# Optimization experiments

Hardware: AMD Instinct MI355X
Metric: run time of the kernel (lower is better)

Reference implementation:

```python
import jax, jax.numpy as jnp
import numpy as np

V = 50257; CTX = 2048; D = 1024; H = 16; L = 8; DH = D // H
B = 2; S = 2048; EPS = 1e-5


def setup_inputs() -> dict:
    key = jax.random.key(0)
    ks = jax.random.split(key, 8)
    s = 0.02
    def n(k, shape):
        return jax.random.normal(k, shape, jnp.float32) * s
    return {
        "x": jax.random.randint(ks[0], (B, S), 0, V),
        "wte": n(ks[1], (V, D)),
        "wpe": n(ks[2], (CTX, D)),
        "ln1_g": jnp.ones((L, D), jnp.float32), "ln1_b": jnp.zeros((L, D), jnp.float32),
        "w_qkv": n(ks[3], (L, D, 3 * D)), "b_qkv": jnp.zeros((L, 3 * D), jnp.float32),
        "w_proj": n(ks[4], (L, D, D)), "b_proj": jnp.zeros((L, D), jnp.float32),
        "ln2_g": jnp.ones((L, D), jnp.float32), "ln2_b": jnp.zeros((L, D), jnp.float32),
        "w_fc": n(ks[5], (L, D, 4 * D)), "b_fc": jnp.zeros((L, 4 * D), jnp.float32),
        "w_cp": n(ks[6], (L, 4 * D, D)), "b_cp": jnp.zeros((L, D), jnp.float32),
        "lnf_g": jnp.ones((D,), jnp.float32), "lnf_b": jnp.zeros((D,), jnp.float32),
        "w_head": n(ks[7], (D, V)),
    }


def layernorm(x, g, b):
    m = x.mean(-1, keepdims=True)
    v = ((x - m) ** 2).mean(-1, keepdims=True)
    return (x - m) * jax.lax.rsqrt(v + EPS) * g + b


def gpt_forward(x, wte, wpe, ln1_g, ln1_b, w_qkv, b_qkv, w_proj, b_proj,
                ln2_g, ln2_b, w_fc, b_fc, w_cp, b_cp, lnf_g, lnf_b, w_head):
    Bx, Sx = x.shape
    h = wte[x] + wpe[:Sx]                       # [B,S,D]
    mask = jnp.tril(jnp.ones((Sx, Sx), bool))   # causal mask
    scale = DH ** -0.5

    def block(h, p):
        g1, b1, wq, bq, wp, bp, g2, b2, wf, bf, wc, bc = p
        y = layernorm(h, g1, b1)
        qkv = y @ wq + bq                        # [B,S,3D]
        q, k, v = jnp.split(qkv, 3, axis=-1)
        q = q.reshape(Bx, Sx, H, DH)
        k = k.reshape(Bx, Sx, H, DH)
        v = v.reshape(Bx, Sx, H, DH)
        att = jnp.einsum('bqhd,bkhd->bhqk', q, k) * scale
        att = jnp.where(mask, att, -jnp.inf)
        att = jax.nn.softmax(att, axis=-1)
        z = jnp.einsum('bhqk,bkhd->bqhd', att, v).reshape(Bx, Sx, D)
        h = h + z @ wp + bp
        y2 = layernorm(h, g2, b2)
        h = h + jax.nn.gelu(y2 @ wf + bf, approximate=False) @ wc + bc
        return h, None

    h, _ = jax.lax.scan(block, h, (ln1_g, ln1_b, w_qkv, b_qkv, w_proj, b_proj,
                                   ln2_g, ln2_b, w_fc, b_fc, w_cp, b_cp))
    h = layernorm(h, lnf_g, lnf_b)
    logits = h[:, -1:, :] @ w_head              # [B,1,V] (last position only)
    return logits


def reference(x, wte, wpe, ln1_g, ln1_b, w_qkv, b_qkv, w_proj, b_proj,
              ln2_g, ln2_b, w_fc, b_fc, w_cp, b_cp, lnf_g, lnf_b, w_head):
    return gpt_forward(x, wte, wpe, ln1_g, ln1_b, w_qkv, b_qkv, w_proj, b_proj,
                       ln2_g, ln2_b, w_fc, b_fc, w_cp, b_cp, lnf_g, lnf_b, w_head)
```

## Files before the change

### kernel.cpp

```cpp
#include <hip/hip_runtime.h>
#include <hip/hip_bf16.h>
#include <math.h>

#define VOCAB 50257
#define CTX 2048
#define DMODEL 1024
#define NHEAD 16
#define NLAYER 8
#define DHEAD 64
#define BATCH 2
#define SEQ 2048
#define NTOK (BATCH * SEQ)

typedef __bf16 bf16x8 __attribute__((ext_vector_type(8)));
typedef float  f32x4  __attribute__((ext_vector_type(4)));
typedef unsigned short ushort4v __attribute__((ext_vector_type(4)));
typedef unsigned short ushort8v __attribute__((ext_vector_type(8)));

__device__ inline void gl_lds16(const void* g, void* l) {
    __builtin_amdgcn_global_load_lds(
        (const __attribute__((address_space(1))) unsigned int*)g,
        (__attribute__((address_space(3))) unsigned int*)l, 16, 0, 0);
}

__device__ inline unsigned short f2bs(float v) {
    __hip_bfloat16 t = __float2bfloat16(v);
    return *(unsigned short*)&t;
}

__device__ void embed_body(int t, const int* __restrict__ x,
                           const float* __restrict__ wte,
                           const float* __restrict__ wpe,
                           float* __restrict__ h) {
    int s = t & (SEQ - 1);
    int tok = x[t];
    const float* pe = wpe + (long)s * DMODEL;
    const float* te = wte + (long)tok * DMODEL;
    float* ph = h + (long)t * DMODEL;
    for (int d = threadIdx.x; d < DMODEL; d += 256)
        ph[d] = te[d] + pe[d];
}

__device__ inline float wave_sum(float v) {
    for (int off = 32; off; off >>= 1) v += __shfl_xor(v, off);
    return v;
}

__global__ void ln_wave(const float* __restrict__ in, unsigned short* __restrict__ out,
                        const float* __restrict__ g, const float* __restrict__ b) {
    const int w = threadIdx.x >> 6, lane = threadIdx.x & 63;
    const int row = blockIdx.x * 4 + w;
    const float* px = in + (long)row * DMODEL;
    f32x4 x[4];
    float s = 0.f;
    #pragma unroll
    for (int i = 0; i < 4; ++i) {
        x[i] = *(const f32x4*)&px[i * 256 + lane * 4];
        s += x[i][0] + x[i][1] + x[i][2] + x[i][3];
    }
    s = wave_sum(s);
    const float mean = s * (1.0f / DMODEL);
    float s2 = 0.f;
    #pragma unroll
    for (int i = 0; i < 4; ++i)
        #pragma unroll
        for (int j = 0; j < 4; ++j) { float d = x[i][j] - mean; s2 += d * d; }
    s2 = wave_sum(s2);
    const float r = 1.0f / sqrtf(s2 * (1.0f / DMODEL) + 1e-5f);
    unsigned short* po = out + (long)row * DMODEL;
    #pragma unroll
    for (int i = 0; i < 4; ++i) {
        const int d0 = i * 256 + lane * 4;
        f32x4 gv = *(const f32x4*)&g[d0];
        f32x4 bv = *(const f32x4*)&b[d0];
        ushort4v pk;
        #pragma unroll
        for (int j = 0; j < 4; ++j)
            pk[j] = f2bs((x[i][j] - mean) * r * gv[j] + bv[j]);
        *(ushort4v*)&po[d0] = pk;
    }
}

__global__ void ln_final(const float* __restrict__ in, float* __restrict__ out,
                         const float* __restrict__ g, const float* __restrict__ b,
                         long row_stride) {
    __shared__ float red[4], red2[4];
    int row = blockIdx.x;
    const float* px = in + (long)row * row_stride;
    float* po = out + (long)row * DMODEL;
    int tid = threadIdx.x;
    int wid = tid >> 6, lane = tid & 63;
    float x[4];
    float s = 0.f;
    #pragma unroll
    for (int i = 0; i < 4; ++i) { x[i] = px[tid + i * 256]; s += x[i]; }
    s = wave_sum(s);
    if (lane == 0) red[wid] = s;
    __syncthreads();
    float mean = (red[0] + red[1] + red[2] + red[3]) * (1.0f / DMODEL);
    float s2 = 0.f;
    #pragma unroll
    for (int i = 0; i < 4; ++i) { float d = x[i] - mean; s2 += d * d; }
    s2 = wave_sum(s2);
    if (lane == 0) red2[wid] = s2;
    __syncthreads();
    float var = (red2[0] + red2[1] + red2[2] + red2[3]) * (1.0f / DMODEL);
    float r = 1.0f / sqrtf(var + 1e-5f);
    #pragma unroll
    for (int i = 0; i < 4; ++i) {
        int d = tid + i * 256;
        po[d] = (x[i] - mean) * r * g[d] + b[d];
    }
}

__device__ void convT_body(char* smem, int kx, int ny, const float* __restrict__ W,
                           unsigned short* __restrict__ WT, int K, int N) {
    float (*t)[65] = (float(*)[65])smem;
    const int k0 = kx * 64, n0 = ny * 64;
    const int tid = threadIdx.x;
    {
        const int krow = tid >> 4, c4 = (tid & 15) * 4;
        #pragma unroll
        for (int p = 0; p < 4; ++p) {
            f32x4 gv = *(const f32x4*)&W[(long)(k0 + p * 16 + krow) * N + n0 + c4];
            #pragma unroll
            for (int j = 0; j < 4; ++j) t[p * 16 + krow][c4 + j] = gv[j];
        }
    }
    __syncthreads();
    {
        const int n = tid >> 3, kl = (tid & 7) * 8;
        #pragma unroll
        for (int p = 0; p < 2; ++p) {
            ushort8v pk;
            #pragma unroll
            for (int j = 0; j < 8; ++j) pk[j] = f2bs(t[kl + j][p * 32 + n]);
            *(ushort8v*)&WT[(long)(n0 + p * 32 + n) * K + k0 + kl] = pk;
        }
    }
}

__device__ void convT_body512(char* smem, int kx, int ny, const float* __restrict__ W,
                              unsigned short* __restrict__ WT, int K, int N) {
    float (*t)[65] = (float(*)[65])smem;
    const int k0 = kx * 64, n0 = ny * 64;
    const int tid = threadIdx.x;
    {
        const int krow = tid >> 4, c4 = (tid & 15) * 4;
        #pragma unroll
        for (int p = 0; p < 2; ++p) {
            f32x4 gv = *(const f32x4*)&W[(long)(k0 + p * 32 + krow) * N + n0 + c4];
            #pragma unroll
            for (int j = 0; j < 4; ++j) t[p * 32 + krow][c4 + j] = gv[j];
        }
    }
    __syncthreads();
    {
        const int n = tid >> 3, kl = (tid & 7) * 8;
        ushort8v pk;
        #pragma unroll
        for (int j = 0; j < 8; ++j) pk[j] = f2bs(t[kl + j][n]);
        *(ushort8v*)&WT[(long)(n0 + n) * K + k0 + kl] = pk;
    }
}

#define STG_A(KS, H) do { \
    const unsigned short* g_ = A + (long)(bm + (H) * 128 + srow) * K + (KS) * 64 + stgch; \
    unsigned short* s_ = LDS + (((KS) & 1) * 2 + (H)) * 8192 + (w * 8) * 64; \
    gl_lds16(g_, s_); gl_lds16(g_ + 64L * K, s_ + 4096); \
} while (0)
#define STG_B(KS, H) do { \
    const unsigned short* g_ = BT + (long)(bn + (H) * 128 + srow) * K + (KS) * 64 + stgch; \
    unsigned short* s_ = LDS + 32768 + (((KS) & 1) * 2 + (H)) * 8192 + (w * 8) * 64; \
    gl_lds16(g_, s_); gl_lds16(g_ + 64L * K, s_ + 4096); \
} while (0)
#define MM2(M_, x0, x1) do { \
    acc[M_][0] = __builtin_amdgcn_mfma_f32_16x16x32_bf16(x0, bfr[0], acc[M_][0], 0, 0, 0); \
    acc[M_][0] = __builtin_amdgcn_mfma_f32_16x16x32_bf16(x1, bfr[1], acc[M_][0], 0, 0, 0); \
    acc[M_][1] = __builtin_amdgcn_mfma_f32_16x16x32_bf16(x0, bfr[2], acc[M_][1], 0, 0, 0); \
    acc[M_][1] = __builtin_amdgcn_mfma_f32_16x16x32_bf16(x1, bfr[3], acc[M_][1], 0, 0, 0); \
    acc[M_][2] = __builtin_amdgcn_mfma_f32_16x16x32_bf16(x0, bfr[4], acc[M_][2], 0, 0, 0); \
    acc[M_][2] = __builtin_amdgcn_mfma_f32_16x16x32_bf16(x1, bfr[5], acc[M_][2], 0, 0, 0); \
    acc[M_][3] = __builtin_amdgcn_mfma_f32_16x16x32_bf16(x0, bfr[6], acc[M_][3], 0, 0, 0); \
    acc[M_][3] = __builtin_amdgcn_mfma_f32_16x16x32_bf16(x1, bfr[7], acc[M_][3], 0, 0, 0); \
} while (0)
#define PHASE(Q, SPAR, STAGE_STMT, TAIL_STMT) do { \
    bf16x8 a00, a01, a10, a11; \
    if (((Q) & 3) == 0) { \
        const unsigned short* Bb_ = lBp[SPAR] + ((wc & 1) * 64 + fr) * 64; \
        bfr[0] = *(const bf16x8*)(Bb_ + rd0);        bfr[1] = *(const bf16x8*)(Bb_ + rd1); \
        bfr[2] = *(const bf16x8*)(Bb_ + 1024 + rd0); bfr[3] = *(const bf16x8*)(Bb_ + 1024 + rd1); \
        bfr[4] = *(const bf16x8*)(Bb_ + 2048 + rd0); bfr[5] = *(const bf16x8*)(Bb_ + 2048 + rd1); \
        bfr[6] = *(const bf16x8*)(Bb_ + 3072 + rd0); bfr[7] = *(const bf16x8*)(Bb_ + 3072 + rd1); \
    } \
    { const unsigned short* Ab_ = lAp[SPAR] + fr * 64; \
      a00 = *(const bf16x8*)(Ab_ + (((Q) & 3) * 2) * 1024 + rd0); \
      a01 = *(const bf16x8*)(Ab_ + (((Q) & 3) * 2) * 1024 + rd1); \
      a10 = *(const bf16x8*)(Ab_ + (((Q) & 3) * 2 + 1) * 1024 + rd0); \
      a11 = *(const bf16x8*)(Ab_ + (((Q) & 3) * 2 + 1) * 1024 + rd1); } \
    STAGE_STMT; \
    __builtin_amdgcn_s_barrier(); \
    asm volatile("s_waitcnt lgkmcnt(0)" ::: "memory"); \
    __builtin_amdgcn_sched_barrier(0); \
    __builtin_amdgcn_s_setprio(1); \
    MM2(((Q) & 3) * 2, a00, a01); \
    MM2(((Q) & 3) * 2 + 1, a10, a11); \
    __builtin_amdgcn_s_setprio(0); \
    TAIL_STMT; \
    __builtin_amdgcn_s_barrier(); \
} while (0)

template<int EPI>
__global__ __launch_bounds__(512, 1)
void mm_mfma256(const unsigned short* __restrict__ A,
                const unsigned short* __restrict__ BT,
                const float* __restrict__ bias,
                void* __restrict__ Cout, int M, int N, int K, int nbx) {
    extern __shared__ unsigned short LDS[];
    const int tid = threadIdx.x;
    const int w = tid >> 6, lane = tid & 63;
    const int wr = w >> 2, wc = w & 3;
    const int nwg = gridDim.x, bid = blockIdx.x;
    const int swz = (bid & 7) * (nwg >> 3) + (bid >> 3);
    const int bm = (swz / nbx) * 256, bn = (swz % nbx) * 256;

    f32x4 acc[8][4];
    #pragma unroll
    for (int m = 0; m < 8; ++m)
        #pragma unroll
        for (int n = 0; n < 4; ++n)
            acc[m][n] = (f32x4){0.f, 0.f, 0.f, 0.f};

    const int fr = lane & 15, kg = lane >> 4;
    const int rd0 = 8 * (kg ^ (lane & 7)), rd1 = 8 * ((kg + 4) ^ (lane & 7));
    const int stgch = 8 * ((lane & 7) ^ (lane >> 3));
    const int srow = w * 8 + (lane >> 3);
    unsigned short* const lAp[2] = { LDS + wr * 8192, LDS + (2 + wr) * 8192 };
    unsigned short* const lBp[2] = { LDS + 32768 + (wc >> 1) * 8192,
                                     LDS + 32768 + (2 + (wc >> 1)) * 8192 };
    bf16x8 bfr[8];

    STG_B(0, 0); STG_B(0, 1); STG_A(0, 0); STG_A(0, 1); STG_B(1, 0); STG_B(1, 1);
    asm volatile("s_waitcnt vmcnt(4)" ::: "memory");
    __builtin_amdgcn_sched_barrier(0);
    __builtin_amdgcn_s_barrier();

    const int T = K >> 7;
    for (int t = 0; t < T; ++t) {
        const int s = 2 * t;
        const bool nl = (t < T - 1);
        PHASE(0, 0, STG_A(s + 1, 0), );
        PHASE(1, 0, STG_A(s + 1, 1), );
        PHASE(2, 0, if (nl) STG_B(s + 2, 0), );
        PHASE(3, 0, if (nl) STG_B(s + 2, 1),
              if (nl) { asm volatile("s_waitcnt vmcnt(4)" ::: "memory"); } else { asm volatile("s_waitcnt vmcnt(0)" ::: "memory"); } __builtin_amdgcn_sched_barrier(0); );
        PHASE(4, 1, if (nl) STG_A(s + 2, 0), );
        PHASE(5, 1, if (nl) STG_A(s + 2, 1), );
        PHASE(6, 1, if (nl) STG_B(s + 3, 0), );
        PHASE(7, 1, if (nl) STG_B(s + 3, 1),
              if (nl) { asm volatile("s_waitcnt vmcnt(4)" ::: "memory"); __builtin_amdgcn_sched_barrier(0); } );
    }

    const int r0 = (lane >> 4) * 4;
    #pragma unroll
    for (int n = 0; n < 4; ++n) {
        int colb = bn + wc * 64 + n * 16;
        float bv = bias[colb + fr];
        #pragma unroll
        for (int m = 0; m < 8; ++m) {
            int rowb = bm + wr * 128 + m * 16 + r0;
            if (EPI == 3) {
                unsigned short* qkvB = (unsigned short*)Cout;
                int which = colb >> 10, hh = (colb & 1023) >> 6, dbase = colb & 63;
                int b_ = rowb >> 11, s_ = rowb & 2047;
                long bh2 = b_ * 16 + hh;
                float v[4];
                #pragma unroll
                for (int r = 0; r < 4; ++r) v[r] = acc[m][n][r] + bv;
                if (which == 2) {
                    ushort4v pk;
                    #pragma unroll
                    for (int r = 0; r < 4; ++r) pk[r] = f2bs(v[r]);
                    *(ushort4v*)&qkvB[8388608L + (bh2 * 64 + dbase + fr) * 2048 + s_] = pk;
                } else {
                    unsigned short* dst = qkvB + (long)which * 4194304L +
                                          (bh2 * 2048 + s_) * 64 + dbase + fr;
                    #pragma unroll
                    for (int r = 0; r < 4; ++r) dst[r * 64] = f2bs(v[r]);
                }
            } else {
                #pragma unroll
                for (int r = 0; r < 4; ++r) {
                    long row = rowb + r, col = colb + fr;
                    float v = acc[m][n][r] + bv;
                    v = 0.5f * v * (1.0f + erff(v * 0.70710678118f));
                    ((__hip_bfloat16*)Cout)[row * N + col] = __float2bfloat16(v);
                }
            }
        }
    }
}

__device__ void n64_body(char* smem, int bx, int by,
                         const unsigned short* __restrict__ A,
                         const unsigned short* __restrict__ BT,
                         const float* __restrict__ bias, const float* __restrict__ R,
                         float* __restrict__ Cout, int M, int N, int K) {
    unsigned short* As = (unsigned short*)smem;
    unsigned short* Bs = As + 2 * 128 * 32;
    const int tid = threadIdx.x;
    const int w = tid >> 6, lane = tid & 63;
    const int bm = by * 128, bn = bx * 64;
    const int wr = (w >> 1) * 64, wc = (w & 1) * 32;

    f32x4 acc[4][2];
    #pragma unroll
    for (int m = 0; m < 4; ++m)
        #pragma unroll
        for (int n = 0; n < 2; ++n)
            acc[m][n] = (f32x4){0.f, 0.f, 0.f, 0.f};

    const int lrow = lane >> 2;
    const int lcol = (lane & 3) * 8;
    const unsigned short* gA = A + (long)(bm + w * 32 + lrow) * K + lcol;
    const unsigned short* gB = BT + (long)(bn + w * 16 + lrow) * K + lcol;

#define N64_STAGE(K0, BB) do { \
    gl_lds16(gA + (K0),          &As[(BB) * 4096 + (w * 32) * 32]); \
    gl_lds16(gA + (K0) + 16 * K, &As[(BB) * 4096 + (w * 32 + 16) * 32]); \
    gl_lds16(gB + (K0),          &Bs[(BB) * 2048 + (w * 16) * 32]); \
} while (0)

    N64_STAGE(0, 0);

    const int T = K >> 5;
    for (int t = 0; t < T; ++t) {
        const int buf = t & 1;
        if (t + 1 < T) {
            N64_STAGE((t + 1) * 32, buf ^ 1);
            asm volatile("s_waitcnt vmcnt(3)" ::: "memory");
        } else {
            asm volatile("s_waitcnt vmcnt(0)" ::: "memory");
        }
        __builtin_amdgcn_sched_barrier(0);
        __builtin_amdgcn_s_barrier();

        bf16x8 a[4], b[2];
        #pragma unroll
        for (int m = 0; m < 4; ++m)
            a[m] = *(const bf16x8*)&As[buf * 4096 + (wr + m * 16 + (lane & 15)) * 32 + (lane >> 4) * 8];
        #pragma unroll
        for (int n = 0; n < 2; ++n)
            b[n] = *(const bf16x8*)&Bs[buf * 2048 + (wc + n * 16 + (lane & 15)) * 32 + (lane >> 4) * 8];
        #pragma unroll
        for (int m = 0; m < 4; ++m)
            #pragma unroll
            for (int n = 0; n < 2; ++n)
                acc[m][n] = __builtin_amdgcn_mfma_f32_16x16x32_bf16(a[m], b[n], acc[m][n], 0, 0, 0);

        __builtin_amdgcn_s_barrier();
    }
#undef N64_STAGE

    const int r0 = (lane >> 4) * 4, cc = lane & 15;
    #pragma unroll
    for (int n = 0; n < 2; ++n) {
        int colb = bn + wc + n * 16;
        float bv = bias[colb + cc];
        #pragma unroll
        for (int m = 0; m < 4; ++m) {
            int rowb = bm + wr + m * 16 + r0;
            #pragma unroll
            for (int r = 0; r < 4; ++r) {
                long row = rowb + r, col = colb + cc;
                float v = acc[m][n][r] + bv + R[row * N + col];
                Cout[row * N + col] = v;
            }
        }
    }
}

__device__ void attn_body(char* smem, int bh, int qb,
                          const unsigned short* __restrict__ qB,
                          const unsigned short* __restrict__ kB,
                          const unsigned short* __restrict__ vT,
                          __hip_bfloat16* __restrict__ z) {
    const int tid = threadIdx.x, w = tid >> 6, lane = tid & 63;
    const int arow = lane & 15, kg = lane >> 4;
    unsigned short* Ks = (unsigned short*)smem;
    unsigned short* Vs = Ks + 128 * 64;
    unsigned short* Ps = Vs + 64 * 128 + w * 16 * 128;

    const long kvbase = (long)bh * (2048 * 64);

    bf16x8 qa[2];
    {
        const unsigned short* q0 = qB + kvbase + (long)(qb + w * 16 + arow) * 64 + kg * 8;
        qa[0] = *(const bf16x8*)(q0);
        qa[1] = *(const bf16x8*)(q0 + 32);
    }

    f32x4 po[4];
    float mrow[4], lrow[4];
    #pragma unroll
    for (int i = 0; i < 4; ++i) {
        po[i] = (f32x4){0.f, 0.f, 0.f, 0.f};
        mrow[i] = -1e30f; lrow[i] = 0.f;
    }

    const int ksrow = lane >> 3;
    const int kschunk = (lane & 7) ^ ksrow;
    const int vsr = lane >> 4;
    const int cmax = qb >> 7;

    for (int c = 0; c <= cmax; ++c) {
        {
            const unsigned short* ks0 = kB + kvbase +
                (long)(c * 128 + w * 16 + ksrow) * 64 + kschunk * 8;
            #pragma unroll
            for (int i = 0; i < 2; ++i)
                gl_lds16(ks0 + (long)i * 8 * 64, &Ks[(w * 16 + i * 8) * 64]);
            #pragma unroll
            for (int i = 0; i < 2; ++i) {
                int d = w * 8 + i * 4 + vsr;
                int sch = (lane & 15) ^ (d & 7);
                gl_lds16(vT + kvbase + (long)d * 2048 + c * 128 + sch * 8,
                         &Vs[(w * 8 + i * 4) * 128]);
            }
        }
        __syncthreads();

        f32x4 s[8];
        #pragma unroll
        for (int n = 0; n < 8; ++n) {
            s[n] = (f32x4){0.f, 0.f, 0.f, 0.f};
            int row = n * 16 + arow, sw = row & 7;
            bf16x8 kb0 = *(const bf16x8*)&Ks[row * 64 + (kg ^ sw) * 8];
            bf16x8 kb1 = *(const bf16x8*)&Ks[row * 64 + ((4 + kg) ^ sw) * 8];
            s[n] = __builtin_amdgcn_mfma_f32_16x16x32_bf16(qa[0], kb0, s[n], 0, 0, 0);
            s[n] = __builtin_amdgcn_mfma_f32_16x16x32_bf16(qa[1], kb1, s[n], 0, 0, 0);
        }

        const bool diag = (c == cmax);
        #pragma unroll
        for (int n = 0; n < 8; ++n)
            #pragma unroll
            for (int r = 0; r < 4; ++r) {
                float v = s[n][r] * 0.125f;
                if (diag) {
                    int key = c * 128 + n * 16 + arow;
                    int qrow = qb + w * 16 + kg * 4 + r;
                    if (key > qrow) v = -1e30f;
                }
                s[n][r] = v;
            }

        #pragma unroll
        for (int r = 0; r < 4; ++r) {
            float rm = s[0][r];
            #pragma unroll
            for (int n = 1; n < 8; ++n) rm = fmaxf(rm, s[n][r]);
            #pragma unroll
            for (int off = 1; off < 16; off <<= 1)
                rm = fmaxf(rm, __shfl_xor(rm, off));
            float mnew = fmaxf(mrow[r], rm);
            float esc = expf(mrow[r] - mnew);
            float rs = 0.f;
            #pragma unroll
            for (int n = 0; n < 8; ++n) {
                float p = expf(s[n][r] - mnew);
                s[n][r] = p;
                rs += p;
            }
            #pragma unroll
            for (int off = 1; off < 16; off <<= 1)
                rs += __shfl_xor(rs, off);
            lrow[r] = lrow[r] * esc + rs;
            #pragma unroll
            for (int dt = 0; dt < 4; ++dt) po[dt][r] *= esc;
            mrow[r] = mnew;
        }

        #pragma unroll
        for (int n = 0; n < 8; ++n) {
            int col = n * 16 + arow;
            int chunk = col >> 3, cw = col & 7;
            #pragma unroll
            for (int r = 0; r < 4; ++r) {
                int row = kg * 4 + r;
                Ps[row * 128 + ((chunk ^ (row & 7)) * 8 + cw)] = f2bs(s[n][r]);
            }
        }

        bf16x8 pa[4];
        #pragma unroll
        for (int ks = 0; ks < 4; ++ks)
            pa[ks] = *(const bf16x8*)&Ps[arow * 128 + (((ks * 4 + kg) ^ (arow & 7)) * 8)];
        #pragma unroll
        for (int dt = 0; dt < 4; ++dt) {
            int vrow = dt * 16 + arow, sw = vrow & 7;
            #pragma unroll
            for (int ks = 0; ks < 4; ++ks) {
                bf16x8 vb = *(const bf16x8*)&Vs[vrow * 128 + (((ks * 4 + kg) ^ sw) * 8)];
                po[dt] = __builtin_amdgcn_mfma_f32_16x16x32_bf16(pa[ks], vb, po[dt], 0, 0, 0);
            }
        }
        __syncthreads();
    }

    const int b_ = bh >> 4, hofs = (bh & 15) * 64;
    #pragma unroll
    for (int dt = 0; dt < 4; ++dt)
        #pragma unroll
        for (int r = 0; r < 4; ++r) {
            long row = (long)b_ * 2048 + qb + w * 16 + kg * 4 + r;
            z[row * 1024 + hofs + dt * 16 + arow] = __float2bfloat16(po[dt][r] / lrow[r]);
        }
}

__global__ __launch_bounds__(256)
void fused_embed_convT(const int* __restrict__ x, const float* __restrict__ wte,
                       const float* __restrict__ wpe, float* __restrict__ h,
                       const float* __restrict__ W, unsigned short* __restrict__ WT,
                       int K, int N, int nEmb) {
    extern __shared__ char smem[];
    int bid = blockIdx.x;
    if (bid < nEmb) {
        embed_body(bid, x, wte, wpe, h);
    } else {
        int r = bid - nEmb, kt = K >> 6;
        convT_body(smem, r % kt, r / kt, W, WT, K, N);
    }
}

__global__ __launch_bounds__(512)
void fused_attn_convT2(const unsigned short* __restrict__ qB,
                       const unsigned short* __restrict__ kB,
                       const unsigned short* __restrict__ vT,
                       __hip_bfloat16* __restrict__ z,
                       const float* __restrict__ W1, unsigned short* __restrict__ WT1,
                       int K1, int N1, int n1,
                       const float* __restrict__ W2, unsigned short* __restrict__ WT2,
                       int K2, int N2, int nAttn) {
    extern __shared__ char smem[];
    int bid = blockIdx.x;
    if (bid < nAttn) {
        int bh = bid & 31;
        int qblk = 15 - (bid >> 5);
        attn_body(smem, bh, qblk * 128, qB, kB, vT, z);
    } else if (bid < nAttn + n1) {
        int r = bid - nAttn, kt = K1 >> 6;
        convT_body512(smem, r % kt, r / kt, W1, WT1, K1, N1);
    } else {
        int r = bid - nAttn - n1, kt = K2 >> 6;
        convT_body512(smem, r % kt, r / kt, W2, WT2, K2, N2);
    }
}

__global__ __launch_bounds__(256)
void fused_n64_convT(const unsigned short* __restrict__ A,
                     const unsigned short* __restrict__ BT,
                     const float* __restrict__ bias, const float* __restrict__ R,
                     float* __restrict__ Cout, int M, int N, int K, int nbx,
                     const float* __restrict__ W2, unsigned short* __restrict__ WT2,
                     int K2, int N2, int nMM) {
    extern __shared__ char smem[];
    int bid = blockIdx.x;
    if (bid < nMM) {
        n64_body(smem, bid % nbx, bid / nbx, A, BT, bias, R, Cout, M, N, K);
    } else {
        int r = bid - nMM, kt = K2 >> 6;
        convT_body(smem, r % kt, r / kt, W2, WT2, K2, N2);
    }
}

__global__ void head_kernel(const float* __restrict__ hl, const float* __restrict__ W,
                            float* __restrict__ out) {
    __shared__ float hs[2 * DMODEL];
    int tid = threadIdx.x;
    #pragma unroll
    for (int i = 0; i < 8; ++i) hs[tid + i * 256] = hl[tid + i * 256];
    __syncthreads();
    int v = blockIdx.x * 256 + tid;
    if (v >= VOCAB) return;
    float a0 = 0.f, a1 = 0.f;
    for (int d = 0; d < DMODEL; ++d) {
        float wv = W[(long)d * VOCAB + v];
        a0 += hs[d] * wv;
        a1 += hs[DMODEL + d] * wv;
    }
    out[v] = a0;
    out[VOCAB + v] = a1;
}

extern "C" void kernel_launch(void* const* d_in, const int* in_sizes, int n_in,
                              void* d_out, int out_size, void* d_ws, size_t ws_size,
                              hipStream_t stream) {
    const int*   x      = (const int*)  d_in[0];
    const float* wte    = (const float*)d_in[1];
    const float* wpe    = (const float*)d_in[2];
    const float* ln1_g  = (const float*)d_in[3];
    const float* ln1_b  = (const float*)d_in[4];
    const float* w_qkv  = (const float*)d_in[5];
    const float* b_qkv  = (const float*)d_in[6];
    const float* w_proj = (const float*)d_in[7];
    const float* b_proj = (const float*)d_in[8];
    const float* ln2_g  = (const float*)d_in[9];
    const float* ln2_b  = (const float*)d_in[10];
    const float* w_fc   = (const float*)d_in[11];
    const float* b_fc   = (const float*)d_in[12];
    const float* w_cp   = (const float*)d_in[13];
    const float* b_cp   = (const float*)d_in[14];
    const float* lnf_g  = (const float*)d_in[15];
    const float* lnf_b  = (const float*)d_in[16];
    const float* w_head = (const float*)d_in[17];
    float* out = (float*)d_out;

    char* ws = (char*)d_ws;
    float*          h     = (float*)ws;
    unsigned short* qkvB  = (unsigned short*)(ws + (16L << 20));
    unsigned short* y_bf  = (unsigned short*)(ws + (40L << 20));
    __hip_bfloat16* z_bf  = (__hip_bfloat16*)(ws + (48L << 20));
    unsigned short* fc_bf = (unsigned short*)(ws + (56L << 20));
    unsigned short* wT_a  = (unsigned short*)(ws + (88L << 20));
    unsigned short* wT_b  = (unsigned short*)(ws + (97L << 20));
    unsigned short* wT_c  = (unsigned short*)(ws + (106L << 20));
    unsigned short* wT_q  = (unsigned short*)(ws + (115L << 20));
    float*          hl    = (float*)(ws + (124L << 20));

    const int SM_CONV = 16640;
    const int SM_ATTN = 65536;
    const int SM_N64  = 24576;

    fused_embed_convT<<<4096 + 768, 256, SM_CONV, stream>>>(
        x, wte, wpe, h, w_qkv, wT_q, 1024, 3072, 4096);

    for (int l = 0; l < NLAYER; ++l) {
        ln_wave<<<NTOK / 4, 256, 0, stream>>>(h, y_bf, ln1_g + l * DMODEL, ln1_b + l * DMODEL);

        mm_mfma256<3><<<192, 512, 131072, stream>>>(
            y_bf, wT_q, b_qkv + l * 3072, qkvB, NTOK, 3072, 1024, 12);

        fused_attn_convT2<<<512 + 256 + 1024, 512, SM_ATTN, stream>>>(
            qkvB, qkvB + 4194304L, qkvB + 8388608L, z_bf,
            w_proj + (long)l * DMODEL * DMODEL, wT_b, 1024, 1024, 256,
            w_cp + (long)l * 4096 * DMODEL, wT_c, 4096, 1024, 512);

        fused_n64_convT<<<512 + 1024, 256, SM_N64, stream>>>(
            (const unsigned short*)z_bf, wT_b, b_proj + l * DMODEL, h, h,
            NTOK, 1024, 1024, 16,
            w_fc + (long)l * DMODEL * 4096, wT_a, 1024, 4096, 512);

        ln_wave<<<NTOK / 4, 256, 0, stream>>>(h, y_bf, ln2_g + l * DMODEL, ln2_b + l * DMODEL);

        mm_mfma256<2><<<256, 512, 131072, stream>>>(
            y_bf, wT_a, b_fc + l * 4096, fc_bf, NTOK, 4096, 1024, 16);

        int nConv = (l + 1 < NLAYER) ? 768 : 0;
        fused_n64_convT<<<512 + nConv, 256, SM_N64, stream>>>(
            fc_bf, wT_c, b_cp + l * DMODEL, h, h, NTOK, 1024, 4096, 16,
            w_qkv + (long)(l + 1) * DMODEL * 3072, wT_q, 1024, 3072, 512);
    }

    ln_final<<<BATCH, 256, 0, stream>>>(h + (long)(SEQ - 1) * DMODEL, hl,
                                        lnf_g, lnf_b, (long)SEQ * DMODEL);
    head_kernel<<<(VOCAB + 255) / 256, 256, 0, stream>>>(hl, w_head, out);
}
```

Baseline: 2.275 ms.

## Overlap w_proj conversion with QKV GEMM and triple-buffer n64 GEMM

Moves the w_proj fp32-to-bf16 transpose blocks out of the attention launch and appends them to the QKV GEMM launch, so they fill CUs left idle by that GEMM's 192-block grid. Separately, the n64 GEMM's LDS staging goes from double to triple buffering, with two tiles prefetched ahead and a matching vmcnt wait. The extra convert blocks in the 256-tile GEMM launch each reserve 128KB of LDS, which limits how many can run at once. The larger LDS footprint for n64 may also reduce occupancy.

Measured after the change: 2.269 ms. No clear change (-0.3%).

```diff
diff --git a/kernel.cpp b/kernel.cpp
--- a/kernel.cpp
+++ b/kernel.cpp
@@ -211,16 +211,14 @@
 } while (0)
 
 template<int EPI>
-__global__ __launch_bounds__(512, 1)
-void mm_mfma256(const unsigned short* __restrict__ A,
-                const unsigned short* __restrict__ BT,
-                const float* __restrict__ bias,
-                void* __restrict__ Cout, int M, int N, int K, int nbx) {
-    extern __shared__ unsigned short LDS[];
+__device__ void mm256_body(unsigned short* LDS, int bid, int nwg,
+                           const unsigned short* __restrict__ A,
+                           const unsigned short* __restrict__ BT,
+                           const float* __restrict__ bias,
+                           void* __restrict__ Cout, int M, int N, int K, int nbx) {
     const int tid = threadIdx.x;
     const int w = tid >> 6, lane = tid & 63;
     const int wr = w >> 2, wc = w & 3;
-    const int nwg = gridDim.x, bid = blockIdx.x;
     const int swz = (bid & 7) * (nwg >> 3) + (bid >> 3);
     const int bm = (swz / nbx) * 256, bn = (swz % nbx) * 256;
 
@@ -301,13 +299,41 @@
     }
 }
 
+template<int EPI>
+__global__ __launch_bounds__(512, 1)
+void mm_mfma256(const unsigned short* __restrict__ A,
+                const unsigned short* __restrict__ BT,
+                const float* __restrict__ bias,
+                void* __restrict__ Cout, int M, int N, int K, int nbx) {
+    extern __shared__ unsigned short LDS[];
+    mm256_body<EPI>(LDS, blockIdx.x, gridDim.x, A, BT, bias, Cout, M, N, K, nbx);
+}
+
+template<int EPI>
+__global__ __launch_bounds__(512, 1)
+void fused_mm256_convT(const unsigned short* __restrict__ A,
+                       const unsigned short* __restrict__ BT,
+                       const float* __restrict__ bias,
+                       void* __restrict__ Cout, int M, int N, int K, int nbx,
+                       const float* __restrict__ W2, unsigned short* __restrict__ WT2,
+                       int K2, int N2, int nMM) {
+    extern __shared__ unsigned short LDS[];
+    int bid = blockIdx.x;
+    if (bid < nMM) {
+        mm256_body<EPI>(LDS, bid, nMM, A, BT, bias, Cout, M, N, K, nbx);
+    } else {
+        int r = bid - nMM, kt = K2 >> 6;
+        convT_body512((char*)LDS, r % kt, r / kt, W2, WT2, K2, N2);
+    }
+}
+
 __device__ void n64_body(char* smem, int bx, int by,
                          const unsigned short* __restrict__ A,
                          const unsigned short* __restrict__ BT,
                          const float* __restrict__ bias, const float* __restrict__ R,
                          float* __restrict__ Cout, int M, int N, int K) {
     unsigned short* As = (unsigned short*)smem;
-    unsigned short* Bs = As + 2 * 128 * 32;
+    unsigned short* Bs = As + 3 * 128 * 32;
     const int tid = threadIdx.x;
     const int w = tid >> 6, lane = tid & 63;
     const int bm = by * 128, bn = bx * 64;
@@ -331,13 +357,16 @@
     gl_lds16(gB + (K0),          &Bs[(BB) * 2048 + (w * 16) * 32]); \
 } while (0)
 
+    const int T = K >> 5;
     N64_STAGE(0, 0);
-
-    const int T = K >> 5;
+    if (T > 1) N64_STAGE(32, 1);
+
     for (int t = 0; t < T; ++t) {
-        const int buf = t & 1;
-        if (t + 1 < T) {
-            N64_STAGE((t + 1) * 32, buf ^ 1);
+        const int buf = t % 3;
+        if (t + 2 < T) {
+            N64_STAGE((t + 2) * 32, (t + 2) % 3);
+            asm volatile("s_waitcnt vmcnt(6)" ::: "memory");
+        } else if (t + 1 < T) {
             asm volatile("s_waitcnt vmcnt(3)" ::: "memory");
         } else {
             asm volatile("s_waitcnt vmcnt(0)" ::: "memory");
@@ -534,25 +563,20 @@
 }
 
 __global__ __launch_bounds__(512)
-void fused_attn_convT2(const unsigned short* __restrict__ qB,
-                       const unsigned short* __restrict__ kB,
-                       const unsigned short* __restrict__ vT,
-                       __hip_bfloat16* __restrict__ z,
-                       const float* __restrict__ W1, unsigned short* __restrict__ WT1,
-                       int K1, int N1, int n1,
-                       const float* __restrict__ W2, unsigned short* __restrict__ WT2,
-                       int K2, int N2, int nAttn) {
+void fused_attn_convT(const unsigned short* __restrict__ qB,
+                      const unsigned short* __restrict__ kB,
+                      const unsigned short* __restrict__ vT,
+                      __hip_bfloat16* __restrict__ z,
+                      const float* __restrict__ W2, unsigned short* __restrict__ WT2,
+                      int K2, int N2, int nAttn) {
     extern __shared__ char smem[];
     int bid = blockIdx.x;
     if (bid < nAttn) {
         int bh = bid & 31;
         int qblk = 15 - (bid >> 5);
         attn_body(smem, bh, qblk * 128, qB, kB, vT, z);
-    } else if (bid < nAttn + n1) {
-        int r = bid - nAttn, kt = K1 >> 6;
-        convT_body512(smem, r % kt, r / kt, W1, WT1, K1, N1);
     } else {
-        int r = bid - nAttn - n1, kt = K2 >> 6;
+        int r = bid - nAttn, kt = K2 >> 6;
         convT_body512(smem, r % kt, r / kt, W2, WT2, K2, N2);
     }
 }
@@ -630,7 +654,7 @@
 
     const int SM_CONV = 16640;
     const int SM_ATTN = 65536;
-    const int SM_N64  = 24576;
+    const int SM_N64  = 36864;
 
     fused_embed_convT<<<4096 + 768, 256, SM_CONV, stream>>>(
         x, wte, wpe, h, w_qkv, wT_q, 1024, 3072, 4096);
@@ -638,12 +662,12 @@
     for (int l = 0; l < NLAYER; ++l) {
         ln_wave<<<NTOK / 4, 256, 0, stream>>>(h, y_bf, ln1_g + l * DMODEL, ln1_b + l * DMODEL);
 
-        mm_mfma256<3><<<192, 512, 131072, stream>>>(
-            y_bf, wT_q, b_qkv + l * 3072, qkvB, NTOK, 3072, 1024, 12);
-
-        fused_attn_convT2<<<512 + 256 + 1024, 512, SM_ATTN, stream>>>(
+        fused_mm256_convT<3><<<192 + 256, 512, 131072, stream>>>(
+            y_bf, wT_q, b_qkv + l * 3072, qkvB, NTOK, 3072, 1024, 12,
+            w_proj + (long)l * DMODEL * DMODEL, wT_b, 1024, 1024, 192);
+
+        fused_attn_convT<<<512 + 1024, 512, SM_ATTN, stream>>>(
             qkvB, qkvB + 4194304L, qkvB + 8388608L, z_bf,
-            w_proj + (long)l * DMODEL * DMODEL, wT_b, 1024, 1024, 256,
             w_cp + (long)l * 4096 * DMODEL, wT_c, 4096, 1024, 512);
 
         fused_n64_convT<<<512 + 1024, 256, SM_N64, stream>>>(
```
